# Optimization experiments

Measured on AMD Instinct MI355X. Metric: run time of the kernel, lower is better.

## Reference

```python
import jax, jax.numpy as jnp
import numpy as np

CHAN = 24
INNER = 64
GROUPS = 8
M = 5
LAM = 1e-4
MAX_ITER = 25
BETA = 1.0
EPS = 1e-5
B, HH, WW = 128, 32, 32


def conv2d(x, w, b=None):
    # NCHW, OIHW, 3x3 SAME conv (padding = kernel//2)
    y = jax.lax.conv_general_dilated(x, w, (1, 1), 'SAME',
                                     dimension_numbers=('NCHW', 'OIHW', 'NCHW'))
    if b is not None:
        y = y + b[None, :, None, None]
    return y


def group_norm(x, g, b):
    bsz, c, h, w = x.shape
    xg = x.reshape(bsz, GROUPS, c // GROUPS, h, w)
    mu = xg.mean(axis=(2, 3, 4), keepdims=True)
    var = xg.var(axis=(2, 3, 4), keepdims=True)
    xn = ((xg - mu) / jnp.sqrt(var + EPS)).reshape(bsz, c, h, w)
    return xn * g[None, :, None, None] + b[None, :, None, None]


def batch_norm(x, g, b):
    # training-mode batch statistics over (N, H, W)
    mu = x.mean(axis=(0, 2, 3), keepdims=True)
    var = x.var(axis=(0, 2, 3), keepdims=True)
    return (x - mu) / jnp.sqrt(var + EPS) * g[None, :, None, None] + b[None, :, None, None]


def resnet_f(p, z, x):
    c1w, g1g, g1b, c2w, g2g, g2b, g3g, g3b = p
    y = group_norm(jax.nn.relu(conv2d(z, c1w)), g1g, g1b)
    return group_norm(jax.nn.relu(z + group_norm(x + conv2d(y, c2w), g2g, g2b)), g3g, g3b)


def anderson(f, x0):
    # Anderson acceleration, fixed MAX_ITER iterations (no host-sync tol break).
    bsz = x0.shape[0]
    d = x0.size // bsz
    X = jnp.zeros((bsz, M, d), x0.dtype)
    Fm = jnp.zeros((bsz, M, d), x0.dtype)
    f0 = f(x0).reshape(bsz, -1)
    X = X.at[:, 0].set(x0.reshape(bsz, -1))
    Fm = Fm.at[:, 0].set(f0)
    X = X.at[:, 1].set(f0)
    Fm = Fm.at[:, 1].set(f(f0.reshape(x0.shape)).reshape(bsz, -1))
    for k in range(2, MAX_ITER):
        n = min(k, M)
        G = Fm[:, :n] - X[:, :n]                       # [b, n, d]
        Hm = jnp.zeros((bsz, n + 1, n + 1), x0.dtype)
        Hm = Hm.at[:, 0, 1:].set(1.0).at[:, 1:, 0].set(1.0)
        Hm = Hm.at[:, 1:, 1:].set(jnp.einsum('bnd,bmd->bnm', G, G)
                                  + LAM * jnp.eye(n, dtype=x0.dtype)[None])
        yv = jnp.zeros((bsz, n + 1, 1), x0.dtype).at[:, 0, 0].set(1.0)
        alpha = jnp.linalg.solve(Hm, yv)[:, 1:, 0]     # [b, n]
        xnew = (BETA * jnp.einsum('bn,bnd->bd', alpha, Fm[:, :n])
                + (1.0 - BETA) * jnp.einsum('bn,bnd->bd', alpha, X[:, :n]))
        X = X.at[:, k % M].set(xnew)
        Fm = Fm.at[:, k % M].set(f(xnew.reshape(x0.shape)).reshape(bsz, -1))
    return X[:, (MAX_ITER - 1) % M].reshape(x0.shape)


def setup_inputs() -> dict:
    key = jax.random.key(0)
    ks = jax.random.split(key, 8)
    inp = {
        'x': jax.random.normal(ks[0], (B, 3, HH, WW), jnp.float32),
        'pre_conv_w': jax.random.normal(ks[1], (CHAN, 3, 3, 3), jnp.float32) * 0.1,
        'pre_conv_b': jnp.zeros((CHAN,), jnp.float32),
        'pre_bn_g': jnp.ones((CHAN,), jnp.float32),
        'pre_bn_b': jnp.zeros((CHAN,), jnp.float32),
        'f_conv1_w': jax.random.normal(ks[2], (INNER, CHAN, 3, 3), jnp.float32) * 0.01,
        'gn1_g': jnp.ones((INNER,), jnp.float32),
        'gn1_b': jnp.zeros((INNER,), jnp.float32),
        'f_conv2_w': jax.random.normal(ks[3], (CHAN, INNER, 3, 3), jnp.float32) * 0.01,
        'gn2_g': jnp.ones((CHAN,), jnp.float32),
        'gn2_b': jnp.zeros((CHAN,), jnp.float32),
        'gn3_g': jnp.ones((CHAN,), jnp.float32),
        'gn3_b': jnp.zeros((CHAN,), jnp.float32),
        'post_bn_g': jnp.ones((CHAN,), jnp.float32),
        'post_bn_b': jnp.zeros((CHAN,), jnp.float32),
        'fc_w': jax.random.normal(ks[4], (10, CHAN * 4 * 4), jnp.float32) * 0.05,
        'fc_b': jnp.zeros((10,), jnp.float32),
    }
    return inp


def reference(x, pre_conv_w, pre_conv_b, pre_bn_g, pre_bn_b,
              f_conv1_w, gn1_g, gn1_b, f_conv2_w, gn2_g, gn2_b, gn3_g, gn3_b,
              post_bn_g, post_bn_b, fc_w, fc_b):
    # pre: conv + BatchNorm
    xp = batch_norm(conv2d(x, pre_conv_w, pre_conv_b), pre_bn_g, pre_bn_b)
    p = (f_conv1_w, gn1_g, gn1_b, f_conv2_w, gn2_g, gn2_b, gn3_g, gn3_b)
    # DEQ fixed-point solve (eval path: train=False returns the fixed point)
    z_star = anderson(lambda z: resnet_f(p, z, xp), jnp.zeros_like(xp))
    z = resnet_f(p, z_star, xp)
    # post: relu -> BN -> avgpool(8,8) -> flatten -> linear
    h = batch_norm(jax.nn.relu(z), post_bn_g, post_bn_b)
    bsz, c, hh, ww = h.shape
    pooled = h.reshape(bsz, c, hh // 8, 8, ww // 8, 8).mean(axis=(3, 5))  # [B,C,4,4]
    return pooled.reshape(bsz, -1) @ fc_w.T + fc_b
```

## Files before the change

kernel.cpp:

```cpp
#include <hip/hip_runtime.h>
#include <hip/hip_bf16.h>

typedef __hip_bfloat16 bf16;
typedef unsigned short ushortT;
typedef __attribute__((ext_vector_type(8))) short short8;
typedef __attribute__((ext_vector_type(4))) float f32x4;

#define BB 128
#define CHAN 24
#define INNER 64
#define HW 1024
#define DD (CHAN*HW)

constexpr size_t cBD = (size_t)BB*DD;
constexpr size_t cYB = (size_t)BB*INNER*HW;

__device__ __attribute__((aligned(16))) ushortT g_xp[cBD];
__device__ __attribute__((aligned(16))) ushortT g_X[5*cBD];
__device__ __attribute__((aligned(16))) ushortT g_F[5*cBD];
__device__ __attribute__((aligned(16))) ushortT g_G[5*cBD];
__device__ __attribute__((aligned(16))) ushortT g_yb[cYB];
__device__ __attribute__((aligned(16))) ushortT g_tb[cBD];
__device__ __attribute__((aligned(16))) ushortT g_w1m[9*64*32];
__device__ __attribute__((aligned(16))) ushortT g_w2m[9*24*64];
__device__ __attribute__((aligned(16))) float g_stats2a[48];
__device__ __attribute__((aligned(16))) float g_stats2b[48];
__device__ __attribute__((aligned(16))) float g_gn1sum[BB*8*2];
__device__ __attribute__((aligned(16))) float g_gn2sum[BB*24*2];
__device__ __attribute__((aligned(16))) float g_gn3p[BB*4*16];
__device__ __attribute__((aligned(16))) float g_gramp[BB*4*5*5];
__device__ __attribute__((aligned(16))) float g_gram[BB*25];
__device__ __attribute__((aligned(16))) float g_pooled[BB*CHAN*16];
__device__ __attribute__((aligned(16))) float g_params[5120];
__device__ unsigned g_isbf16;

#define P_PCW 0
#define P_PCB 648
#define P_PBG 672
#define P_PBB 696
#define P_G1G 720
#define P_G1B 784
#define P_G2G 848
#define P_G2B 872
#define P_G3G 896
#define P_G3B 920
#define P_POG 944
#define P_POB 968
#define P_FCW 992
#define P_FCB 4832

__device__ __forceinline__ size_t aidx(int b, int icv, int pix){
  return (((size_t)b*3 + icv)*1024 + (size_t)pix)*8;
}
__device__ __forceinline__ float rdin(const void* p, int i){
  if (g_isbf16) return __bfloat162float(((const bf16*)p)[i]);
  return ((const float*)p)[i];
}
__device__ __forceinline__ float b2f(ushortT u){
  unsigned v = ((unsigned)u) << 16;
  return __builtin_bit_cast(float, v);
}
__device__ __forceinline__ ushortT f2b(float f){
  unsigned u = __builtin_bit_cast(unsigned, f);
  u += 0x7FFFu + ((u >> 16) & 1u);
  return (ushortT)(u >> 16);
}
__device__ __forceinline__ void ld24c(const ushortT* base, int b, int pix, float* o){
  #pragma unroll
  for (int icv=0;icv<3;icv++){
    short8 v = *(const short8*)&base[aidx(b,icv,pix)];
    #pragma unroll
    for (int j=0;j<8;j++) o[icv*8+j] = b2f((ushortT)v[j]);
  }
}
__device__ __forceinline__ void st24c(ushortT* base, int b, int pix, const float* i){
  #pragma unroll
  for (int icv=0;icv<3;icv++){
    short8 v;
    #pragma unroll
    for (int j=0;j<8;j++) v[j] = (short)f2b(i[icv*8+j]);
    *(short8*)&base[aidx(b,icv,pix)] = v;
  }
}

__global__ void detect_k(const void* g1g){
  if (threadIdx.x==0 && blockIdx.x==0){
    unsigned u = *(const unsigned*)g1g;
    g_isbf16 = (u == 0x3F803F80u) ? 1u : 0u;
  }
}

__global__ void cvt_params_k(const void* pcw, const void* pcb, const void* pbg, const void* pbb,
                             const void* g1g, const void* g1b, const void* g2g, const void* g2b,
                             const void* g3g, const void* g3b, const void* pog, const void* pob,
                             const void* fcw, const void* fcb){
  int t = threadIdx.x;
  for (int i=t;i<648;i+=256)  g_params[P_PCW+i]=rdin(pcw,i);
  for (int i=t;i<24;i+=256) { g_params[P_PCB+i]=rdin(pcb,i);
                              g_params[P_PBG+i]=rdin(pbg,i);
                              g_params[P_PBB+i]=rdin(pbb,i);
                              g_params[P_G2G+i]=rdin(g2g,i);
                              g_params[P_G2B+i]=rdin(g2b,i);
                              g_params[P_G3G+i]=rdin(g3g,i);
                              g_params[P_G3B+i]=rdin(g3b,i);
                              g_params[P_POG+i]=rdin(pog,i);
                              g_params[P_POB+i]=rdin(pob,i); }
  for (int i=t;i<64;i+=256) { g_params[P_G1G+i]=rdin(g1g,i);
                              g_params[P_G1B+i]=rdin(g1b,i); }
  for (int i=t;i<3840;i+=256) g_params[P_FCW+i]=rdin(fcw,i);
  for (int i=t;i<10;i+=256)   g_params[P_FCB+i]=rdin(fcb,i);
  for (int i=t;i<48;i+=256) { g_stats2a[i]=0.f; g_stats2b[i]=0.f; }
}

__global__ void wtm_k(const void* w1, const void* w2){
  int t = blockIdx.x*256 + threadIdx.x;
  if (t < 9*64*32){
    int ic = t & 31, oc = (t>>5)&63, s9 = t>>11;
    float v = (ic<24) ? rdin(w1, (oc*24+ic)*9 + s9) : 0.f;
    g_w1m[t] = f2b(v);
  }
  int u = t - 9*64*32;
  if (u >= 0 && u < 9*24*64){
    int ic = u & 63; int rest = u >> 6; int oc = rest % 24; int s9 = rest / 24;
    g_w2m[u] = f2b(rdin(w2, (oc*64+ic)*9 + s9));
  }
}

__global__ void zeroX0_k(){
  size_t i = ((size_t)blockIdx.x*256 + threadIdx.x)*8;
  short8 z = {0,0,0,0,0,0,0,0};
  *(short8*)&g_X[i] = z;
  if (blockIdx.x < 8) g_gn1sum[blockIdx.x*256 + threadIdx.x] = 0.f;
}
__global__ void copyF0toX1_k(){
  size_t i = ((size_t)blockIdx.x*256 + threadIdx.x)*8;
  *(short8*)&g_X[cBD + i] = *(const short8*)&g_F[i];
  if (blockIdx.x < 8) g_gn1sum[blockIdx.x*256 + threadIdx.x] = 0.f;
}

__global__ void preconv_k(const void* __restrict__ x){
  int id = blockIdx.x*256 + threadIdx.x;
  int b = id >> 10, pix = id & 1023;
  int yy = pix >> 5, xx = pix & 31;
  float acc[24];
  #pragma unroll
  for (int oc=0;oc<24;oc++) acc[oc] = g_params[P_PCB+oc];
  for (int ic=0; ic<3; ic++)
    for (int ky=0; ky<3; ky++){
      int gy = yy+ky-1; if (gy<0||gy>=32) continue;
      for (int kx=0;kx<3;kx++){
        int gx = xx+kx-1; if (gx<0||gx>=32) continue;
        float v = rdin(x, ((b*3+ic)*32+gy)*32+gx);
        #pragma unroll
        for (int oc=0;oc<24;oc++)
          acc[oc] += v * g_params[P_PCW+(oc*3+ic)*9+ky*3+kx];
      }
    }
  st24c(g_tb, b, pix, acc);
}

template<bool RELU>
__global__ void bnstat2_k(int which){
  const ushortT* src = (which==0) ? g_tb : (g_F + 4*cBD);
  float* dst = (which==0) ? g_stats2a : g_stats2b;
  __shared__ float sRed[48];
  int b = blockIdx.x >> 2, seg = blockIdx.x & 3;
  int t = threadIdx.x;
  if (t < 48) sRed[t] = 0.f;
  __syncthreads();
  int icv = t >> 6, pl = t & 63;
  float p0[8], p1[8];
  #pragma unroll
  for (int e=0;e<8;e++){ p0[e]=0.f; p1[e]=0.f; }
  for (int it=0; it<4; it++){
    int pix = seg*256 + it*64 + pl;
    short8 v = *(const short8*)&src[aidx(b,icv,pix)];
    #pragma unroll
    for (int e=0;e<8;e++){
      float f = b2f((ushortT)v[e]); if (RELU) f = fmaxf(f,0.f);
      p0[e]+=f; p1[e]+=f*f;
    }
  }
  #pragma unroll
  for (int e=0;e<8;e++){
    atomicAdd(&sRed[(icv*8+e)*2],   p0[e]);
    atomicAdd(&sRed[(icv*8+e)*2+1], p1[e]);
  }
  __syncthreads();
  if (t < 48) atomicAdd(&dst[t], sRed[t]);
}

__global__ void bn_apply_k(){
  int id = blockIdx.x*256+threadIdx.x;
  int b = id >> 10, pix = id & 1023;
  const float inv = 1.f/(BB*HW);
  float tv[24], ov[24];
  ld24c(g_tb, b, pix, tv);
  #pragma unroll
  for (int c=0;c<24;c++){
    float mean = g_stats2a[c*2]*inv;
    float var = fmaxf(g_stats2a[c*2+1]*inv - mean*mean, 0.f);
    float rstd = rsqrtf(var + 1e-5f);
    ov[c] = (tv[c]-mean)*rstd*g_params[P_PBG+c] + g_params[P_PBB+c];
  }
  st24c(g_xp, b, pix, ov);
}

__launch_bounds__(256, 2)
__global__ void conv1_k(int s){
  __shared__ ushortT sMem[29312];
  ushortT* sA = sMem;
  ushortT* sW = sMem + 10880;
  const int tid = threadIdx.x;
  const int lane = tid & 63, wv = tid >> 6;
  const int mLane = lane & 15, q = lane >> 4;
  const int b = blockIdx.x >> 2, yt = blockIdx.x & 3;
  const ushortT* __restrict__ Xs = g_X + (size_t)s*cBD;
  if (blockIdx.x < 24) g_gn2sum[blockIdx.x*256 + tid] = 0.f;
  for (int i = tid; i < 1360; i += 256){
    int icv = i & 3, apix = i >> 2;
    int yl = apix / 34, xl = apix - yl*34;
    int gy = yt*8 - 1 + yl, gx = xl - 1;
    short8 v = {0,0,0,0,0,0,0,0};
    if (gy >= 0 && gy < 32 && gx >= 0 && gx < 32 && icv < 3)
      v = *(const short8*)&Xs[aidx(b, icv, gy*32 + gx)];
    *(short8*)&sA[(size_t)(apix*4 + (icv ^ (apix&3)))*8] = v;
  }
  for (int i = tid; i < 2304; i += 256){
    int icv = i & 3, rest = i >> 2;
    int oc = rest & 63, s9 = rest >> 6;
    short8 v = *(const short8*)&g_w1m[(size_t)((s9*64 + oc)*32) + icv*8];
    *(short8*)&sW[(size_t)((s9*64+oc)*4 + (icv ^ (oc&3)))*8] = v;
  }
  __syncthreads();
  f32x4 acc[4][4];
  #pragma unroll
  for (int mt=0;mt<4;mt++)
    #pragma unroll
    for (int nt=0;nt<4;nt++) acc[mt][nt] = (f32x4){0.f,0.f,0.f,0.f};
  for (int s9=0; s9<9; s9++){
    int ky = s9/3, kx = s9 - ky*3;
    short8 bfr[4];
    #pragma unroll
    for (int nt=0;nt<4;nt++){
      int oc = nt*16 + mLane;
      bfr[nt] = *(const short8*)&sW[(size_t)((s9*64+oc)*4 + (q ^ (oc&3)))*8];
    }
    #pragma unroll
    for (int mt=0;mt<4;mt++){
      int g = wv*4+mt;
      int apix = ((g>>1) + ky)*34 + (g&1)*16 + mLane + kx;
      short8 afr = *(const short8*)&sA[(size_t)(apix*4 + (q ^ (apix&3)))*8];
      #pragma unroll
      for (int nt=0;nt<4;nt++)
        acc[mt][nt] = __builtin_amdgcn_mfma_f32_16x16x32_bf16(afr, bfr[nt], acc[mt][nt], 0,0,0);
    }
  }
  __syncthreads();
  ushortT* sOut = sMem;
  #pragma unroll
  for (int mt=0;mt<4;mt++){
    int g = wv*4+mt;
    #pragma unroll
    for (int nt=0;nt<4;nt++){
      int oc = nt*16 + mLane;
      #pragma unroll
      for (int r=0;r<4;r++){
        int pix = (g>>1)*32 + (g&1)*16 + q*4 + r;
        sOut[pix*64 + oc] = f2b(fmaxf(acc[mt][nt][r], 0.f));
      }
    }
  }
  __syncthreads();
  float s0=0.f, s1=0.f;
  size_t gbase = ((size_t)b*1024 + yt*256)*64;
  for (int c = tid; c < 2048; c += 256){
    short8 v = *(const short8*)&sOut[c*8];
    *(short8*)&g_yb[gbase + (size_t)c*8] = v;
    #pragma unroll
    for (int j=0;j<8;j++){ float f = b2f((ushortT)v[j]); s0 += f; s1 += f*f; }
  }
  s0 += __shfl_down(s0,32); s1 += __shfl_down(s1,32);
  s0 += __shfl_down(s0,16); s1 += __shfl_down(s1,16);
  s0 += __shfl_down(s0, 8); s1 += __shfl_down(s1, 8);
  if (lane < 8){
    atomicAdd(&g_gn1sum[(b*8+lane)*2],   s0);
    atomicAdd(&g_gn1sum[(b*8+lane)*2+1], s1);
  }
}

__launch_bounds__(256, 2)
__global__ void conv2_k(){
  __shared__ ushortT sMem[35584];
  __shared__ float sAff[128];
  ushortT* sA = sMem;
  ushortT* sW = sMem + 21760;
  const int tid = threadIdx.x;
  const int lane = tid & 63, wv = tid >> 6;
  const int mLane = lane & 15, q = lane >> 4;
  const int b = blockIdx.x >> 2, yt = blockIdx.x & 3;
  if (tid < 64){
    int c = tid, gr = c>>3;
    float S = g_gn1sum[(b*8+gr)*2], Q = g_gn1sum[(b*8+gr)*2+1];
    float mean = S*(1.f/8192.f);
    float var = fmaxf(Q*(1.f/8192.f) - mean*mean, 0.f);
    float rstd = rsqrtf(var + 1e-5f);
    float sc = rstd*g_params[P_G1G+c];
    sAff[c] = sc; sAff[64+c] = g_params[P_G1B+c] - mean*sc;
  }
  __syncthreads();
  for (int i = tid; i < 2720; i += 256){
    int icv = i & 7, apix = i >> 3;
    int yl = apix / 34, xl = apix - yl*34;
    int gy = yt*8 - 1 + yl, gx = xl - 1;
    short8 v = {0,0,0,0,0,0,0,0};
    if (gy >= 0 && gy < 32 && gx >= 0 && gx < 32){
      short8 raw = *(const short8*)&g_yb[((size_t)b*1024 + gy*32+gx)*64 + icv*8];
      #pragma unroll
      for (int j=0;j<8;j++){
        int c = icv*8+j;
        v[j] = (short)f2b(b2f((ushortT)raw[j])*sAff[c] + sAff[64+c]);
      }
    }
    *(short8*)&sA[(size_t)(apix*8 + (icv ^ (apix&7)))*8] = v;
  }
  for (int i = tid; i < 1728; i += 256){
    int icv = i & 7, rest = i >> 3;
    int oc = rest % 24, s9 = rest / 24;
    short8 v = *(const short8*)&g_w2m[(size_t)((s9*24+oc)*64) + icv*8];
    *(short8*)&sW[(size_t)((s9*24+oc)*8 + (icv ^ (oc&7)))*8] = v;
  }
  __syncthreads();
  f32x4 acc[4][2];
  #pragma unroll
  for (int mt=0;mt<4;mt++){ acc[mt][0]=(f32x4){0.f,0.f,0.f,0.f}; acc[mt][1]=(f32x4){0.f,0.f,0.f,0.f}; }
  const bool nt1ok = (mLane < 8);
  for (int s9=0; s9<9; s9++){
    int ky = s9/3, kx = s9 - ky*3;
    #pragma unroll
    for (int ks=0; ks<2; ks++){
      int ib = ks*4;
      short8 bfr[2];
      { int oc = mLane;
        bfr[0] = *(const short8*)&sW[(size_t)((s9*24+oc)*8 + ((ib+q) ^ (oc&7)))*8]; }
      if (nt1ok){
        int oc = 16 + mLane;
        bfr[1] = *(const short8*)&sW[(size_t)((s9*24+oc)*8 + ((ib+q) ^ (oc&7)))*8];
      } else bfr[1] = (short8){0,0,0,0,0,0,0,0};
      #pragma unroll
      for (int mt=0;mt<4;mt++){
        int g = wv*4+mt;
        int apix = ((g>>1) + ky)*34 + (g&1)*16 + mLane + kx;
        short8 afr = *(const short8*)&sA[(size_t)(apix*8 + ((ib+q) ^ (apix&7)))*8];
        acc[mt][0] = __builtin_amdgcn_mfma_f32_16x16x32_bf16(afr, bfr[0], acc[mt][0], 0,0,0);
        acc[mt][1] = __builtin_amdgcn_mfma_f32_16x16x32_bf16(afr, bfr[1], acc[mt][1], 0,0,0);
      }
    }
  }
  #pragma unroll
  for (int nt=0;nt<2;nt++){
    int oc = nt*16 + mLane;
    bool ok = (oc < 24);
    int icv = oc >> 3, e = oc & 7;
    float s0=0.f, s1=0.f;
    if (ok){
      #pragma unroll
      for (int mt=0;mt<4;mt++){
        int g = wv*4+mt;
        #pragma unroll
        for (int r=0;r<4;r++){
          int pix = (yt*8 + (g>>1))*32 + (g&1)*16 + q*4 + r;
          size_t o = aidx(b, icv, pix) + e;
          float v = acc[mt][nt][r] + b2f(g_xp[o]);
          g_tb[o] = f2b(v);
          s0 += v; s1 += v*v;
        }
      }
    }
    s0 += __shfl_down(s0,32); s1 += __shfl_down(s1,32);
    s0 += __shfl_down(s0,16); s1 += __shfl_down(s1,16);
    if (lane < 16 && ok){
      atomicAdd(&g_gn2sum[(b*24+oc)*2],   s0);
      atomicAdd(&g_gn2sum[(b*24+oc)*2+1], s1);
    }
  }
}

__launch_bounds__(256)
__global__ void fuse_a_k(int s){
  __shared__ float sM2[8], sR2[8], sSc2[24], sSb2[24];
  __shared__ float sRed[64];
  const int b = blockIdx.x>>2, seg = blockIdx.x&3;
  const int t = threadIdx.x;
  if (t < 8){
    float S = g_gn2sum[(b*24+t*3)*2]   + g_gn2sum[(b*24+t*3+1)*2]   + g_gn2sum[(b*24+t*3+2)*2];
    float Q = g_gn2sum[(b*24+t*3)*2+1] + g_gn2sum[(b*24+t*3+1)*2+1] + g_gn2sum[(b*24+t*3+2)*2+1];
    float m = S*(1.f/3072.f);
    sM2[t] = m;
    sR2[t] = rsqrtf(fmaxf(Q*(1.f/3072.f) - m*m, 0.f) + 1e-5f);
  }
  __syncthreads();
  if (t < 24){
    int g = t/3;
    float sc = sR2[g]*g_params[P_G2G+t];
    sSc2[t] = sc; sSb2[t] = g_params[P_G2B+t] - sM2[g]*sc;
  }
  __syncthreads();
  const int pix = seg*256 + t;
  float tv[24], xv[24];
  ld24c(g_tb, b, pix, tv);
  ld24c(g_X + (size_t)s*cBD, b, pix, xv);
  float p0[8], p1[8];
  #pragma unroll
  for (int g=0;g<8;g++){ p0[g]=0.f; p1[g]=0.f; }
  #pragma unroll
  for (int c=0;c<24;c++){
    int g = c/3;
    float v = fmaxf(xv[c] + tv[c]*sSc2[c] + sSb2[c], 0.f);
    p0[g] += v; p1[g] += v*v;
  }
  #pragma unroll
  for (int g=0;g<8;g++){
    for (int off=32;off>0;off>>=1){ p0[g]+=__shfl_down(p0[g],off,64); p1[g]+=__shfl_down(p1[g],off,64); }
  }
  int lane = t&63, wv = t>>6;
  if (lane==0){
    #pragma unroll
    for (int g=0;g<8;g++){ sRed[wv*16+g*2]=p0[g]; sRed[wv*16+g*2+1]=p1[g]; }
  }
  __syncthreads();
  if (t < 16){
    g_gn3p[(b*4+seg)*16 + t] = sRed[t]+sRed[16+t]+sRed[32+t]+sRed[48+t];
  }
}

__launch_bounds__(256)
__global__ void fuse_b_k(int s, int nv){
  __shared__ float sM2[8], sR2[8], sM3[8], sR3[8];
  __shared__ float sSc2[24], sSb2[24], sSc3[24], sSb3[24];
  __shared__ float sRedG[4][5];
  const int b = blockIdx.x>>2, seg = blockIdx.x&3;
  const int t = threadIdx.x;
  if (t < 8){
    float S = g_gn2sum[(b*24+t*3)*2]   + g_gn2sum[(b*24+t*3+1)*2]   + g_gn2sum[(b*24+t*3+2)*2];
    float Q = g_gn2sum[(b*24+t*3)*2+1] + g_gn2sum[(b*24+t*3+1)*2+1] + g_gn2sum[(b*24+t*3+2)*2+1];
    float m = S*(1.f/3072.f);
    sM2[t] = m;
    sR2[t] = rsqrtf(fmaxf(Q*(1.f/3072.f) - m*m, 0.f) + 1e-5f);
    float S3 = g_gn3p[(b*4+0)*16+t*2]   + g_gn3p[(b*4+1)*16+t*2]
             + g_gn3p[(b*4+2)*16+t*2]   + g_gn3p[(b*4+3)*16+t*2];
    float Q3 = g_gn3p[(b*4+0)*16+t*2+1] + g_gn3p[(b*4+1)*16+t*2+1]
             + g_gn3p[(b*4+2)*16+t*2+1] + g_gn3p[(b*4+3)*16+t*2+1];
    float m3 = S3*(1.f/3072.f);
    sM3[t] = m3;
    sR3[t] = rsqrtf(fmaxf(Q3*(1.f/3072.f) - m3*m3, 0.f) + 1e-5f);
  }
  __syncthreads();
  if (t < 24){
    int g = t/3;
    float sc2 = sR2[g]*g_params[P_G2G+t];
    sSc2[t] = sc2; sSb2[t] = g_params[P_G2B+t] - sM2[g]*sc2;
    float sc3 = sR3[g]*g_params[P_G3G+t];
    sSc3[t] = sc3; sSb3[t] = g_params[P_G3B+t] - sM3[g]*sc3;
  }
  __syncthreads();
  const int pix = seg*256 + t;
  float tv[24], xv[24], fv[24], gl[24];
  ld24c(g_tb, b, pix, tv);
  ld24c(g_X + (size_t)s*cBD, b, pix, xv);
  #pragma unroll
  for (int c=0;c<24;c++){
    float v = fmaxf(xv[c] + tv[c]*sSc2[c] + sSb2[c], 0.f);
    fv[c] = v*sSc3[c] + sSb3[c];
    float g = fv[c] - xv[c];
    gl[c] = b2f(f2b(g));
  }
  st24c(g_F + (size_t)s*cBD, b, pix, fv);
  st24c(g_G + (size_t)s*cBD, b, pix, gl);
  if (nv == 0) return;
  float part[5];
  #pragma unroll
  for (int j=0;j<5;j++) part[j]=0.f;
  #pragma unroll
  for (int j=0;j<5;j++){
    if (j>=nv) continue;
    float acc=0.f;
    if (j==s){
      #pragma unroll
      for (int c=0;c<24;c++) acc += gl[c]*gl[c];
    } else {
      float gv[24];
      ld24c(g_G + (size_t)j*cBD, b, pix, gv);
      #pragma unroll
      for (int c=0;c<24;c++) acc += gl[c]*gv[c];
    }
    part[j]=acc;
  }
  int lane = t&63, wv = t>>6;
  #pragma unroll
  for (int j=0;j<5;j++){
    float v = part[j];
    for (int off=32;off>0;off>>=1) v += __shfl_down(v,off,64);
    if (lane==0 && j<nv) sRedG[wv][j] = v;
  }
  __syncthreads();
  if (t < 5 && t < nv){
    float v = sRedG[0][t]+sRedG[1][t]+sRedG[2][t]+sRedG[3][t];
    g_gramp[((b*4+seg)*5 + s)*5 + t] = v;
  }
}

template<int N>
__device__ __forceinline__ void chol_alpha(const float Kf[5][5], float* alpha){
  double K[N][N];
  #pragma unroll
  for (int i=0;i<N;i++)
    #pragma unroll
    for (int j=0;j<N;j++)
      K[i][j] = (double)Kf[i][j] + (i==j ? 1e-4 : 0.0);
  #pragma unroll
  for (int c=0;c<N;c++){
    double d = K[c][c];
    #pragma unroll
    for (int k2=0;k2<c;k2++) d -= K[c][k2]*K[c][k2];
    d = sqrt(fmax(d, 1e-300));
    K[c][c] = d;
    double inv = 1.0/d;
    #pragma unroll
    for (int r=c+1;r<N;r++){
      double v = K[r][c];
      #pragma unroll
      for (int k2=0;k2<c;k2++) v -= K[r][k2]*K[c][k2];
      K[r][c] = v*inv;
    }
  }
  double y[N];
  #pragma unroll
  for (int i=0;i<N;i++){
    double v = 1.0;
    #pragma unroll
    for (int j=0;j<i;j++) v -= K[i][j]*y[j];
    y[i] = v / K[i][i];
  }
  double w[N];
  #pragma unroll
  for (int i=N-1;i>=0;i--){
    double v = y[i];
    #pragma unroll
    for (int j=i+1;j<N;j++) v -= K[j][i]*w[j];
    w[i] = v / K[i][i];
  }
  double sum = 0.0;
  #pragma unroll
  for (int i=0;i<N;i++) sum += w[i];
  double invs = 1.0/sum;
  #pragma unroll
  for (int i=0;i<N;i++) alpha[i] = (float)(w[i]*invs);
}

__global__ void xns_k(int s, int n, int rA, int nvA, int rB, int nvB){
  __shared__ float sAlpha[5];
  if (blockIdx.x < 8) g_gn1sum[blockIdx.x*256 + threadIdx.x] = 0.f;
  const int b = blockIdx.x >> 2, ch = blockIdx.x & 3;
  const int t = threadIdx.x;
  if (t == 0){
    float Kf[5][5];
    for (int i=0;i<n;i++)
      for (int j=0;j<n;j++) Kf[i][j] = g_gram[b*25 + i*5 + j];
    for (int j=0;j<nvA;j++){
      float v = g_gramp[((b*4+0)*5 + rA)*5 + j] + g_gramp[((b*4+1)*5 + rA)*5 + j]
              + g_gramp[((b*4+2)*5 + rA)*5 + j] + g_gramp[((b*4+3)*5 + rA)*5 + j];
      Kf[rA][j] = v; Kf[j][rA] = v;
    }
    if (rB >= 0){
      for (int j=0;j<nvB;j++){
        float v = g_gramp[((b*4+0)*5 + rB)*5 + j] + g_gramp[((b*4+1)*5 + rB)*5 + j]
                + g_gramp[((b*4+2)*5 + rB)*5 + j] + g_gramp[((b*4+3)*5 + rB)*5 + j];
        Kf[rB][j] = v; Kf[j][rB] = v;
      }
    }
    if (ch == 0){
      for (int j=0;j<nvA;j++){ g_gram[b*25+rA*5+j]=Kf[rA][j]; g_gram[b*25+j*5+rA]=Kf[rA][j]; }
      if (rB >= 0)
        for (int j=0;j<nvB;j++){ g_gram[b*25+rB*5+j]=Kf[rB][j]; g_gram[b*25+j*5+rB]=Kf[rB][j]; }
    }
    float al[5];
    if (n==2) chol_alpha<2>(Kf, al);
    else if (n==3) chol_alpha<3>(Kf, al);
    else if (n==4) chol_alpha<4>(Kf, al);
    else chol_alpha<5>(Kf, al);
    for (int j=0;j<n;j++) sAlpha[j] = al[j];
  }
  __syncthreads();
  float a[5];
  for (int j=0;j<n;j++) a[j] = sAlpha[j];
  const size_t base = (size_t)b*DD + (size_t)ch*6144;
  #pragma unroll
  for (int i=0;i<3;i++){
    size_t off = base + (size_t)i*2048 + (size_t)t*8;
    float acc[8];
    #pragma unroll
    for (int e=0;e<8;e++) acc[e]=0.f;
    for (int j=0;j<n;j++){
      short8 f = *(const short8*)&g_F[(size_t)j*cBD + off];
      float aj = a[j];
      #pragma unroll
      for (int e=0;e<8;e++) acc[e] += aj*b2f((ushortT)f[e]);
    }
    short8 o;
    #pragma unroll
    for (int e=0;e<8;e++) o[e] = (short)f2b(acc[e]);
    *(short8*)&g_X[(size_t)s*cBD + off] = o;
  }
}

__global__ void post_pool_k(){
  int i = blockIdx.x*256+threadIdx.x; if (i >= BB*CHAN*16) return;
  const ushortT* z = g_F + 4*cBD;
  int pw = i&3, ph=(i>>2)&3, c=(i>>4)%CHAN, bi=i/(CHAN*16);
  int icv = c>>3, e = c&7;
  float inv = 1.f/(BB*HW);
  float mean = g_stats2b[c*2]*inv;
  float var = fmaxf(g_stats2b[c*2+1]*inv - mean*mean, 0.f);
  float rstd = rsqrtf(var + 1e-5f);
  float gg=g_params[P_POG+c], bv=g_params[P_POB+c];
  float s=0.f;
  for (int dy=0;dy<8;dy++)
    for (int dx=0;dx<8;dx++){
      int pix = (ph*8+dy)*32 + pw*8+dx;
      float v = fmaxf(b2f(z[aidx(bi,icv,pix) + e]), 0.f);
      s += (v-mean)*rstd*gg + bv;
    }
  g_pooled[i] = s*(1.f/64.f);
}

__global__ void fc_k(void* __restrict__ out){
  int i = blockIdx.x*256+threadIdx.x; if (i>=BB*10) return;
  int j=i%10, bi=i/10;
  float s = g_params[P_FCB+j];
  for (int k=0;k<384;k++) s += g_pooled[bi*384+k]*g_params[P_FCW+j*384+k];
  if (g_isbf16) ((bf16*)out)[i] = __float2bfloat16(s);
  else ((float*)out)[i] = s;
}

extern "C" void kernel_launch(void* const* d_in, const int* in_sizes, int n_in,
                              void* d_out, int out_size, void* d_ws, size_t ws_size,
                              hipStream_t stream){
  const void* x   = d_in[0];
  const void* pcw = d_in[1];
  const void* pcb = d_in[2];
  const void* pbg = d_in[3];
  const void* pbb = d_in[4];
  const void* w1  = d_in[5];
  const void* g1g = d_in[6];
  const void* g1b = d_in[7];
  const void* w2  = d_in[8];
  const void* g2g = d_in[9];
  const void* g2b = d_in[10];
  const void* g3g = d_in[11];
  const void* g3b = d_in[12];
  const void* pog = d_in[13];
  const void* pob = d_in[14];
  const void* fcw = d_in[15];
  const void* fcb = d_in[16];
  (void)d_ws; (void)ws_size;

  const int gPix = (int)(BB*HW/256);

  auto feval = [&](int s, int nv){
    conv1_k<<<512,256,0,stream>>>(s);
    conv2_k<<<512,256,0,stream>>>();
    fuse_a_k<<<512,256,0,stream>>>(s);
    fuse_b_k<<<512,256,0,stream>>>(s, nv);
  };

  detect_k<<<1,64,0,stream>>>(g1g);
  cvt_params_k<<<1,256,0,stream>>>(pcw,pcb,pbg,pbb,g1g,g1b,g2g,g2b,g3g,g3b,pog,pob,fcw,fcb);
  wtm_k<<<126,256,0,stream>>>(w1, w2);

  preconv_k<<<gPix,256,0,stream>>>(x);
  bnstat2_k<false><<<512,192,0,stream>>>(0);
  bn_apply_k<<<gPix,256,0,stream>>>();

  zeroX0_k<<<1536,256,0,stream>>>();
  feval(0, 1);
  copyF0toX1_k<<<1536,256,0,stream>>>();
  feval(1, 2);

  for (int k=2;k<25;k++){
    int n = k<5 ? k : 5;
    int s = k%5;
    int nv = (k+1<5)?(k+1):5;
    if (k==2) xns_k<<<512,256,0,stream>>>(s, 2, 0, 1, 1, 2);
    else      xns_k<<<512,256,0,stream>>>(s, n, (k-1)%5, n, -1, 0);
    feval(s, (k<24) ? nv : 0);
  }

  bnstat2_k<true><<<512,192,0,stream>>>(1);
  post_pool_k<<<(BB*CHAN*16+255)/256,256,0,stream>>>();
  fc_k<<<(BB*10+255)/256,256,0,stream>>>(d_out);
}
```

Baseline: 1.592 ms.

## Fuse group-norm-3 stats and output kernels into one per-sample block

New measurement: 1.602 ms. Within noise of the previous version (+0.6%).

```diff
diff --git a/kernel.cpp b/kernel.cpp
--- a/kernel.cpp
+++ b/kernel.cpp
@@ -27,7 +27,6 @@
 __device__ __attribute__((aligned(16))) float g_stats2b[48];
 __device__ __attribute__((aligned(16))) float g_gn1sum[BB*8*2];
 __device__ __attribute__((aligned(16))) float g_gn2sum[BB*24*2];
-__device__ __attribute__((aligned(16))) float g_gn3p[BB*4*16];
 __device__ __attribute__((aligned(16))) float g_gramp[BB*4*5*5];
 __device__ __attribute__((aligned(16))) float g_gram[BB*25];
 __device__ __attribute__((aligned(16))) float g_pooled[BB*CHAN*16];
@@ -386,127 +385,91 @@
   }
 }
 
-__launch_bounds__(256)
-__global__ void fuse_a_k(int s){
-  __shared__ float sM2[8], sR2[8], sSc2[24], sSb2[24];
-  __shared__ float sRed[64];
-  const int b = blockIdx.x>>2, seg = blockIdx.x&3;
-  const int t = threadIdx.x;
-  if (t < 8){
-    float S = g_gn2sum[(b*24+t*3)*2]   + g_gn2sum[(b*24+t*3+1)*2]   + g_gn2sum[(b*24+t*3+2)*2];
-    float Q = g_gn2sum[(b*24+t*3)*2+1] + g_gn2sum[(b*24+t*3+1)*2+1] + g_gn2sum[(b*24+t*3+2)*2+1];
-    float m = S*(1.f/3072.f);
-    sM2[t] = m;
-    sR2[t] = rsqrtf(fmaxf(Q*(1.f/3072.f) - m*m, 0.f) + 1e-5f);
-  }
-  __syncthreads();
+__launch_bounds__(1024, 1)
+__global__ void fuse_k(int s, int nv){
+  __shared__ float sS3[16], sGrow[5], sAff[96];
+  const int b = blockIdx.x, t = threadIdx.x;
+  const int lane = t & 63;
+  if (t < 16) sS3[t] = 0.f;
+  else if (t < 21) sGrow[t-16] = 0.f;
   if (t < 24){
     int g = t/3;
-    float sc = sR2[g]*g_params[P_G2G+t];
-    sSc2[t] = sc; sSb2[t] = g_params[P_G2B+t] - sM2[g]*sc;
-  }
-  __syncthreads();
-  const int pix = seg*256 + t;
+    float S = g_gn2sum[(b*24+g*3)*2]   + g_gn2sum[(b*24+g*3+1)*2]   + g_gn2sum[(b*24+g*3+2)*2];
+    float Q = g_gn2sum[(b*24+g*3)*2+1] + g_gn2sum[(b*24+g*3+1)*2+1] + g_gn2sum[(b*24+g*3+2)*2+1];
+    float m = S*(1.f/3072.f);
+    float rs = rsqrtf(fmaxf(Q*(1.f/3072.f) - m*m, 0.f) + 1e-5f);
+    float sc = rs*g_params[P_G2G+t];
+    sAff[t] = sc; sAff[24+t] = g_params[P_G2B+t] - m*sc;
+  }
+  __syncthreads();
   float tv[24], xv[24];
-  ld24c(g_tb, b, pix, tv);
-  ld24c(g_X + (size_t)s*cBD, b, pix, xv);
+  ld24c(g_tb, b, t, tv);
+  ld24c(g_X + (size_t)s*cBD, b, t, xv);
   float p0[8], p1[8];
   #pragma unroll
   for (int g=0;g<8;g++){ p0[g]=0.f; p1[g]=0.f; }
   #pragma unroll
   for (int c=0;c<24;c++){
     int g = c/3;
-    float v = fmaxf(xv[c] + tv[c]*sSc2[c] + sSb2[c], 0.f);
+    float v = fmaxf(xv[c] + tv[c]*sAff[c] + sAff[24+c], 0.f);
     p0[g] += v; p1[g] += v*v;
   }
   #pragma unroll
   for (int g=0;g<8;g++){
     for (int off=32;off>0;off>>=1){ p0[g]+=__shfl_down(p0[g],off,64); p1[g]+=__shfl_down(p1[g],off,64); }
   }
-  int lane = t&63, wv = t>>6;
   if (lane==0){
     #pragma unroll
-    for (int g=0;g<8;g++){ sRed[wv*16+g*2]=p0[g]; sRed[wv*16+g*2+1]=p1[g]; }
-  }
-  __syncthreads();
-  if (t < 16){
-    g_gn3p[(b*4+seg)*16 + t] = sRed[t]+sRed[16+t]+sRed[32+t]+sRed[48+t];
-  }
-}
-
-__launch_bounds__(256)
-__global__ void fuse_b_k(int s, int nv){
-  __shared__ float sM2[8], sR2[8], sM3[8], sR3[8];
-  __shared__ float sSc2[24], sSb2[24], sSc3[24], sSb3[24];
-  __shared__ float sRedG[4][5];
-  const int b = blockIdx.x>>2, seg = blockIdx.x&3;
-  const int t = threadIdx.x;
-  if (t < 8){
-    float S = g_gn2sum[(b*24+t*3)*2]   + g_gn2sum[(b*24+t*3+1)*2]   + g_gn2sum[(b*24+t*3+2)*2];
-    float Q = g_gn2sum[(b*24+t*3)*2+1] + g_gn2sum[(b*24+t*3+1)*2+1] + g_gn2sum[(b*24+t*3+2)*2+1];
-    float m = S*(1.f/3072.f);
-    sM2[t] = m;
-    sR2[t] = rsqrtf(fmaxf(Q*(1.f/3072.f) - m*m, 0.f) + 1e-5f);
-    float S3 = g_gn3p[(b*4+0)*16+t*2]   + g_gn3p[(b*4+1)*16+t*2]
-             + g_gn3p[(b*4+2)*16+t*2]   + g_gn3p[(b*4+3)*16+t*2];
-    float Q3 = g_gn3p[(b*4+0)*16+t*2+1] + g_gn3p[(b*4+1)*16+t*2+1]
-             + g_gn3p[(b*4+2)*16+t*2+1] + g_gn3p[(b*4+3)*16+t*2+1];
-    float m3 = S3*(1.f/3072.f);
-    sM3[t] = m3;
-    sR3[t] = rsqrtf(fmaxf(Q3*(1.f/3072.f) - m3*m3, 0.f) + 1e-5f);
+    for (int g=0;g<8;g++){ atomicAdd(&sS3[g*2], p0[g]); atomicAdd(&sS3[g*2+1], p1[g]); }
   }
   __syncthreads();
   if (t < 24){
     int g = t/3;
-    float sc2 = sR2[g]*g_params[P_G2G+t];
-    sSc2[t] = sc2; sSb2[t] = g_params[P_G2B+t] - sM2[g]*sc2;
-    float sc3 = sR3[g]*g_params[P_G3G+t];
-    sSc3[t] = sc3; sSb3[t] = g_params[P_G3B+t] - sM3[g]*sc3;
-  }
-  __syncthreads();
-  const int pix = seg*256 + t;
-  float tv[24], xv[24], fv[24], gl[24];
-  ld24c(g_tb, b, pix, tv);
-  ld24c(g_X + (size_t)s*cBD, b, pix, xv);
+    float m3 = sS3[g*2]*(1.f/3072.f);
+    float rs3 = rsqrtf(fmaxf(sS3[g*2+1]*(1.f/3072.f) - m3*m3, 0.f) + 1e-5f);
+    float sc3 = rs3*g_params[P_G3G+t];
+    sAff[48+t] = sc3; sAff[72+t] = g_params[P_G3B+t] - m3*sc3;
+  }
+  __syncthreads();
+  float fv[24], gl[24];
   #pragma unroll
   for (int c=0;c<24;c++){
-    float v = fmaxf(xv[c] + tv[c]*sSc2[c] + sSb2[c], 0.f);
-    fv[c] = v*sSc3[c] + sSb3[c];
-    float g = fv[c] - xv[c];
-    gl[c] = b2f(f2b(g));
-  }
-  st24c(g_F + (size_t)s*cBD, b, pix, fv);
-  st24c(g_G + (size_t)s*cBD, b, pix, gl);
-  if (nv == 0) return;
-  float part[5];
-  #pragma unroll
-  for (int j=0;j<5;j++) part[j]=0.f;
-  #pragma unroll
-  for (int j=0;j<5;j++){
-    if (j>=nv) continue;
-    float acc=0.f;
-    if (j==s){
-      #pragma unroll
-      for (int c=0;c<24;c++) acc += gl[c]*gl[c];
-    } else {
-      float gv[24];
-      ld24c(g_G + (size_t)j*cBD, b, pix, gv);
-      #pragma unroll
-      for (int c=0;c<24;c++) acc += gl[c]*gv[c];
-    }
-    part[j]=acc;
-  }
-  int lane = t&63, wv = t>>6;
-  #pragma unroll
-  for (int j=0;j<5;j++){
-    float v = part[j];
-    for (int off=32;off>0;off>>=1) v += __shfl_down(v,off,64);
-    if (lane==0 && j<nv) sRedG[wv][j] = v;
-  }
-  __syncthreads();
-  if (t < 5 && t < nv){
-    float v = sRedG[0][t]+sRedG[1][t]+sRedG[2][t]+sRedG[3][t];
-    g_gramp[((b*4+seg)*5 + s)*5 + t] = v;
+    float v = fmaxf(xv[c] + tv[c]*sAff[c] + sAff[24+c], 0.f);
+    fv[c] = v*sAff[48+c] + sAff[72+c];
+    gl[c] = b2f(f2b(fv[c] - xv[c]));
+  }
+  st24c(g_F + (size_t)s*cBD, b, t, fv);
+  st24c(g_G + (size_t)s*cBD, b, t, gl);
+  if (nv > 0){
+    float part[5];
+    #pragma unroll
+    for (int j=0;j<5;j++) part[j]=0.f;
+    #pragma unroll
+    for (int j=0;j<5;j++){
+      if (j>=nv) continue;
+      float acc=0.f;
+      if (j==s){
+        #pragma unroll
+        for (int c=0;c<24;c++) acc += gl[c]*gl[c];
+      } else {
+        float gv[24];
+        ld24c(g_G + (size_t)j*cBD, b, t, gv);
+        #pragma unroll
+        for (int c=0;c<24;c++) acc += gl[c]*gv[c];
+      }
+      part[j]=acc;
+    }
+    #pragma unroll
+    for (int j=0;j<5;j++){
+      float v = part[j];
+      for (int off=32;off>0;off>>=1) v += __shfl_down(v,off,64);
+      if (lane==0 && j<nv) atomicAdd(&sGrow[j], v);
+    }
+  }
+  __syncthreads();
+  if (nv > 0 && t < 20){
+    int seg = t/5, j = t%5;
+    g_gramp[((b*4+seg)*5 + s)*5 + j] = (seg==0 && j<nv) ? sGrow[j] : 0.f;
   }
 }
 
@@ -670,8 +633,7 @@
   auto feval = [&](int s, int nv){
     conv1_k<<<512,256,0,stream>>>(s);
     conv2_k<<<512,256,0,stream>>>();
-    fuse_a_k<<<512,256,0,stream>>>(s);
-    fuse_b_k<<<512,256,0,stream>>>(s, nv);
+    fuse_k<<<128,1024,0,stream>>>(s, nv);
   };
 
   detect_k<<<1,64,0,stream>>>(g1g);
```
